# Optimization experiments

Hardware: AMD Instinct MI355X
Metric: run time of the kernel (lower is better)

The kernel has to match this reference:

```python
import jax, jax.numpy as jnp
import numpy as np

B, NF, V, D, NI = 16384, 26, 100000, 16, 13
HID = [512, 256, 128, 64, 1]

def setup_inputs() -> dict:
    key = jax.random.key(0)
    ks = jax.random.split(key, 24)
    x_int = jax.random.normal(ks[0], (B, NI), dtype=jnp.float32)
    x_cat = jax.random.randint(ks[1], (B, NF), 0, V, dtype=jnp.int64)
    emb_tables = jax.random.normal(ks[2], (NF, V, D), dtype=jnp.float32) * 0.01
    lin_tables = jax.random.normal(ks[3], (NF, V, 1), dtype=jnp.float32) * 0.01
    W_num = jax.random.normal(ks[4], (NI, 1), dtype=jnp.float32) * 0.1
    b_num = jnp.zeros((1,), dtype=jnp.float32)
    bias = jnp.zeros((1,), dtype=jnp.float32)
    dims = [NF * D + NI] + HID  # 429 -> 512 -> 256 -> 128 -> 64 -> 1
    mlp = {}
    for li in range(5):
        fan_in = dims[li]
        mlp[f'W{li+1}'] = jax.random.normal(ks[5 + 2*li], (dims[li], dims[li+1]), dtype=jnp.float32) / np.sqrt(fan_in)
        mlp[f'b{li+1}'] = jnp.zeros((dims[li+1],), dtype=jnp.float32)
    return dict(x_int=x_int, x_cat=x_cat, emb_tables=emb_tables, lin_tables=lin_tables,
                W_num=W_num, b_num=b_num, bias=bias, **mlp)

def reference(x_int, x_cat, emb_tables, lin_tables, W_num, b_num, bias,
              W1, b1, W2, b2, W3, b3, W4, b4, W5, b5):
    feat_idx = jnp.arange(NF)[None, :]                 # [1, NF]
    emb = emb_tables[feat_idx, x_cat]                  # [B, NF, D] fused gather
    # FM second-order interaction
    sum_emb = jnp.sum(emb, axis=1)                     # [B, D]
    square_of_sum = sum_emb ** 2
    sum_of_square = jnp.sum(emb ** 2, axis=1)
    fm_score = 0.5 * jnp.sum(square_of_sum - sum_of_square, axis=1, keepdims=True)  # [B,1]
    # linear terms
    lin_cat_score = jnp.sum(lin_tables[feat_idx, x_cat], axis=1)  # [B,1]
    lin_num_score = x_int @ W_num + b_num                          # [B,1]
    # deep MLP (dropout is identity at inference)
    deep_in = jnp.concatenate([emb.reshape(emb.shape[0], -1), x_int], axis=1)  # [B, NF*D+NI]
    h = jax.nn.relu(deep_in @ W1 + b1)
    h = jax.nn.relu(h @ W2 + b2)
    h = jax.nn.relu(h @ W3 + b3)
    h = jax.nn.relu(h @ W4 + b4)
    deep_score = h @ W5 + b5                                       # [B,1]
    return bias + lin_cat_score + lin_num_score + fm_score + deep_score
```

## Files before the change

kernel.cpp:

```cpp
#include <hip/hip_runtime.h>
#include <hip/hip_bf16.h>
#include <stdint.h>

typedef __bf16 bf16x8 __attribute__((ext_vector_type(8)));
typedef float  f32x4  __attribute__((ext_vector_type(4)));

#define NROWS 16384
#define NFEAT 26
#define VOCAB 100000

template<int KPAD, int KREAL, int N, int NCT, int WS>
__device__ __forceinline__ void mlp_layer(const float* __restrict__ W,
                                          const float* __restrict__ bias,
                                          const __bf16* Ain, __bf16* Aout,
                                          int w, int lane) {
  constexpr int LDA = KPAD + 8, LDO = N + 8;
  constexpr int KSAFE = (KREAL / 32) * 32;
  const int lrow = lane & 15;
  const int kg = (lane >> 4) * 8;

  f32x4 acc[NCT][4];
  #pragma unroll
  for (int j = 0; j < NCT; ++j)
    #pragma unroll
    for (int m = 0; m < 4; ++m)
      #pragma unroll
      for (int i = 0; i < 4; ++i) acc[j][m][i] = 0.f;

  int col[NCT];
  #pragma unroll
  for (int j = 0; j < NCT; ++j) col[j] = (w + j * WS) * 16 + lrow;

  auto step = [&](int k0, bool clamp) {
    bf16x8 af[4];
    #pragma unroll
    for (int m = 0; m < 4; ++m)
      af[m] = *(const bf16x8*)(Ain + (m * 16 + lrow) * LDA + k0 + kg);
    #pragma unroll
    for (int j = 0; j < NCT; ++j) {
      bf16x8 bf;
      #pragma unroll
      for (int i = 0; i < 8; ++i) {
        int k = k0 + kg + i;
        float v = (!clamp || k < KREAL) ? W[(size_t)k * N + col[j]] : 0.f;
        bf[i] = (__bf16)v;
      }
      #pragma unroll
      for (int m = 0; m < 4; ++m)
        acc[j][m] = __builtin_amdgcn_mfma_f32_16x16x32_bf16(af[m], bf, acc[j][m], 0, 0, 0);
    }
  };

  for (int k0 = 0; k0 < KSAFE; k0 += 32) step(k0, false);
  if constexpr (KSAFE < KPAD) step(KSAFE, true);

  const int rbase = (lane >> 4) * 4;
  #pragma unroll
  for (int j = 0; j < NCT; ++j) {
    float bv = bias[col[j]];
    #pragma unroll
    for (int m = 0; m < 4; ++m)
      #pragma unroll
      for (int i = 0; i < 4; ++i) {
        float v = acc[j][m][i] + bv;
        v = fmaxf(v, 0.f);
        Aout[(m * 16 + rbase + i) * LDO + col[j]] = (__bf16)v;
      }
  }
}

__global__ __launch_bounds__(1024) void k_fused(
    const float* __restrict__ x_int,
    const int*   __restrict__ x_cat,
    const float* __restrict__ emb,
    const float* __restrict__ lin,
    const float* __restrict__ W_num,
    const float* __restrict__ b_num,
    const float* __restrict__ bias0,
    const float* __restrict__ W1, const float* __restrict__ b1,
    const float* __restrict__ W2, const float* __restrict__ b2,
    const float* __restrict__ W3, const float* __restrict__ b3,
    const float* __restrict__ W4, const float* __restrict__ b4,
    const float* __restrict__ W5, const float* __restrict__ b5,
    float* __restrict__ out) {
  __shared__ __align__(16) char smem[125184];
  __bf16* A0 = (__bf16*)smem;
  __bf16* A1 = (__bf16*)(smem + 58368);
  int* s_idx = (int*)(smem + 58368);
  float* s_part = (float*)(smem + 124928);

  const int t = threadIdx.x;
  const int row0 = blockIdx.x * 64;
  const int w = t >> 6, lane = t & 63;

  for (int i = t; i < 64 * NFEAT; i += 1024) {
    int r = i / NFEAT, f = i - r * NFEAT;
    s_idx[i] = x_cat[(size_t)(row0 + r) * NFEAT + f];
  }
  __syncthreads();

  {
    const float pbias = bias0[0] + b_num[0];
    const int r = t >> 4, d = t & 15;
    float sum = 0.f, sumsq = 0.f;
    #pragma unroll
    for (int f = 0; f < NFEAT; ++f) {
      int idx = s_idx[r * NFEAT + f];
      float e = emb[((size_t)f * VOCAB + idx) * 16 + d];
      sum += e; sumsq += e * e;
      A0[r * 456 + f * 16 + d] = (__bf16)e;
    }
    float xv = (d < 13) ? x_int[(size_t)(row0 + r) * 13 + d] : 0.f;
    A0[r * 456 + 416 + d] = (__bf16)xv;
    A0[r * 456 + 432 + d] = (__bf16)0.f;

    float lin_s = lin[(size_t)d * VOCAB + s_idx[r * NFEAT + d]];
    if (d < NFEAT - 16)
      lin_s += lin[(size_t)(d + 16) * VOCAB + s_idx[r * NFEAT + d + 16]];
    float lin_num = (d < 13) ? xv * W_num[d] : 0.f;

    float red = 0.5f * (sum * sum - sumsq) + lin_s + lin_num;
    #pragma unroll
    for (int off = 1; off < 16; off <<= 1) red += __shfl_xor(red, off, 16);
    if (d == 0) s_part[r] = red + pbias;
  }
  __syncthreads();

  mlp_layer<448, 429, 512, 2, 16>(W1, b1, A0, A1, w, lane);
  __syncthreads();
  mlp_layer<512, 512, 256, 1, 16>(W2, b2, A1, A0, w, lane);
  __syncthreads();
  if (w < 8) mlp_layer<256, 256, 128, 1, 8>(W3, b3, A0, A1, w, lane);
  __syncthreads();
  if (w < 4) mlp_layer<128, 128, 64, 1, 4>(W4, b4, A1, A0, w, lane);
  __syncthreads();

  {
    const int r = t >> 4, g = t & 15;
    float s = 0.f;
    #pragma unroll
    for (int i = 0; i < 4; ++i)
      s += (float)A0[r * 72 + g * 4 + i] * W5[g * 4 + i];
    #pragma unroll
    for (int off = 1; off < 16; off <<= 1) s += __shfl_xor(s, off, 16);
    if (g == 0) out[row0 + r] = s + b5[0] + s_part[r];
  }
}

extern "C" void kernel_launch(void* const* d_in, const int* in_sizes, int n_in,
                              void* d_out, int out_size, void* d_ws, size_t ws_size,
                              hipStream_t stream) {
  const float* x_int = (const float*)d_in[0];
  const int*   x_cat = (const int*)d_in[1];
  const float* emb   = (const float*)d_in[2];
  const float* lin   = (const float*)d_in[3];
  const float* W_num = (const float*)d_in[4];
  const float* b_num = (const float*)d_in[5];
  const float* bias  = (const float*)d_in[6];
  const float* W1 = (const float*)d_in[7];  const float* b1 = (const float*)d_in[8];
  const float* W2 = (const float*)d_in[9];  const float* b2 = (const float*)d_in[10];
  const float* W3 = (const float*)d_in[11]; const float* b3 = (const float*)d_in[12];
  const float* W4 = (const float*)d_in[13]; const float* b4 = (const float*)d_in[14];
  const float* W5 = (const float*)d_in[15]; const float* b5 = (const float*)d_in[16];
  float* out = (float*)d_out;

  k_fused<<<NROWS / 64, 1024, 0, stream>>>(x_int, x_cat, emb, lin, W_num, b_num, bias,
                                           W1, b1, W2, b2, W3, b3, W4, b4, W5, b5,
                                           out);
}
```

Baseline: 46.46 us.

## Interleave embedding gather with first MLP layer in feature chunks

The embedding gather and the first MLP layer now run chunk by chunk: each chunk of four features (64 columns) is written to shared memory, then fed to the bf16 MFMA accumulation for layer 1. Meanwhile the next chunk's gather is prefetched with 16-byte vector loads. The aim is to hide the latency of the random embedding reads behind matrix-core work, instead of finishing the whole gather before layer 1 starts. The FM and linear reductions are rebuilt around the new thread mapping. The cost is seven block-wide barriers inside the loop and more live registers.

New measurement: 44.17 us. 1.05x faster.

```diff
diff --git a/kernel.cpp b/kernel.cpp
--- a/kernel.cpp
+++ b/kernel.cpp
@@ -3,6 +3,7 @@
 #include <stdint.h>
 
 typedef __bf16 bf16x8 __attribute__((ext_vector_type(8)));
+typedef __bf16 bf16x4 __attribute__((ext_vector_type(4)));
 typedef float  f32x4  __attribute__((ext_vector_type(4)));
 
 #define NROWS 16384
@@ -15,7 +16,6 @@
                                           const __bf16* Ain, __bf16* Aout,
                                           int w, int lane) {
   constexpr int LDA = KPAD + 8, LDO = N + 8;
-  constexpr int KSAFE = (KREAL / 32) * 32;
   const int lrow = lane & 15;
   const int kg = (lane >> 4) * 8;
 
@@ -31,28 +31,22 @@
   #pragma unroll
   for (int j = 0; j < NCT; ++j) col[j] = (w + j * WS) * 16 + lrow;
 
-  auto step = [&](int k0, bool clamp) {
+  for (int k0 = 0; k0 < KREAL; k0 += 32) {
     bf16x8 af[4];
     #pragma unroll
     for (int m = 0; m < 4; ++m)
       af[m] = *(const bf16x8*)(Ain + (m * 16 + lrow) * LDA + k0 + kg);
     #pragma unroll
     for (int j = 0; j < NCT; ++j) {
-      bf16x8 bf;
-      #pragma unroll
-      for (int i = 0; i < 8; ++i) {
-        int k = k0 + kg + i;
-        float v = (!clamp || k < KREAL) ? W[(size_t)k * N + col[j]] : 0.f;
-        bf[i] = (__bf16)v;
-      }
+      bf16x8 bw;
+      #pragma unroll
+      for (int i = 0; i < 8; ++i)
+        bw[i] = (__bf16)W[(size_t)(k0 + kg + i) * N + col[j]];
       #pragma unroll
       for (int m = 0; m < 4; ++m)
-        acc[j][m] = __builtin_amdgcn_mfma_f32_16x16x32_bf16(af[m], bf, acc[j][m], 0, 0, 0);
-    }
-  };
-
-  for (int k0 = 0; k0 < KSAFE; k0 += 32) step(k0, false);
-  if constexpr (KSAFE < KPAD) step(KSAFE, true);
+        acc[j][m] = __builtin_amdgcn_mfma_f32_16x16x32_bf16(af[m], bw, acc[j][m], 0, 0, 0);
+    }
+  }
 
   const int rbase = (lane >> 4) * 4;
   #pragma unroll
@@ -92,6 +86,7 @@
   const int t = threadIdx.x;
   const int row0 = blockIdx.x * 64;
   const int w = t >> 6, lane = t & 63;
+  const int lrow = lane & 15, kg = (lane >> 4) * 8;
 
   for (int i = t; i < 64 * NFEAT; i += 1024) {
     int r = i / NFEAT, f = i - r * NFEAT;
@@ -99,35 +94,127 @@
   }
   __syncthreads();
 
-  {
-    const float pbias = bias0[0] + b_num[0];
-    const int r = t >> 4, d = t & 15;
-    float sum = 0.f, sumsq = 0.f;
-    #pragma unroll
-    for (int f = 0; f < NFEAT; ++f) {
-      int idx = s_idx[r * NFEAT + f];
-      float e = emb[((size_t)f * VOCAB + idx) * 16 + d];
-      sum += e; sumsq += e * e;
-      A0[r * 456 + f * 16 + d] = (__bf16)e;
-    }
-    float xv = (d < 13) ? x_int[(size_t)(row0 + r) * 13 + d] : 0.f;
-    A0[r * 456 + 416 + d] = (__bf16)xv;
-    A0[r * 456 + 432 + d] = (__bf16)0.f;
-
-    float lin_s = lin[(size_t)d * VOCAB + s_idx[r * NFEAT + d]];
-    if (d < NFEAT - 16)
-      lin_s += lin[(size_t)(d + 16) * VOCAB + s_idx[r * NFEAT + d + 16]];
-    float lin_num = (d < 13) ? xv * W_num[d] : 0.f;
-
-    float red = 0.5f * (sum * sum - sumsq) + lin_s + lin_num;
-    #pragma unroll
-    for (int off = 1; off < 16; off <<= 1) red += __shfl_xor(red, off, 16);
-    if (d == 0) s_part[r] = red + pbias;
-  }
-  __syncthreads();
-
-  mlp_layer<448, 429, 512, 2, 16>(W1, b1, A0, A1, w, lane);
-  __syncthreads();
+  const int r = t >> 4, d = t & 15;
+  const int g = d >> 2, q = d & 3;
+
+  float lin_s = 0.f;
+  if (d < 13) {
+    lin_s = lin[(size_t)d * VOCAB + s_idx[r * NFEAT + d]]
+          + lin[(size_t)(d + 13) * VOCAB + s_idx[r * NFEAT + d + 13]]
+          + x_int[(size_t)(row0 + r) * 13 + d] * W_num[d];
+  }
+  float xv[4] = {0.f, 0.f, 0.f, 0.f};
+  if (d >= 8 && d < 12) {
+    int base = (d - 8) * 4;
+    #pragma unroll
+    for (int i = 0; i < 4; ++i)
+      if (base + i < 13) xv[i] = x_int[(size_t)(row0 + r) * 13 + base + i];
+  }
+
+  f32x4 acc[2][4];
+  #pragma unroll
+  for (int j = 0; j < 2; ++j)
+    #pragma unroll
+    for (int m = 0; m < 4; ++m)
+      #pragma unroll
+      for (int i = 0; i < 4; ++i) acc[j][m][i] = 0.f;
+  const int colL1[2] = { w * 16 + lrow, (w + 16) * 16 + lrow };
+
+  float fsum[4] = {0.f,0.f,0.f,0.f}, fsq[4] = {0.f,0.f,0.f,0.f};
+  f32x4 cur;
+  {
+    int idx = s_idx[r * NFEAT + g];
+    cur = *(const f32x4*)(emb + ((size_t)g * VOCAB + idx) * 16 + q * 4);
+  }
+
+  #pragma unroll
+  for (int c = 0; c < 7; ++c) {
+    f32x4 nxt;
+    if (c < 6) {
+      int fc = 4 * (c + 1) + g;
+      if (fc < NFEAT) {
+        int idx = s_idx[r * NFEAT + fc];
+        nxt = *(const f32x4*)(emb + ((size_t)fc * VOCAB + idx) * 16 + q * 4);
+      }
+    }
+    const int colbase = c * 64 + g * 16 + q * 4;
+    if (4 * c + g < NFEAT) {
+      bf16x4 pk;
+      #pragma unroll
+      for (int i = 0; i < 4; ++i) {
+        fsum[i] += cur[i]; fsq[i] += cur[i] * cur[i];
+        pk[i] = (__bf16)cur[i];
+      }
+      *(bf16x4*)(A0 + r * 456 + colbase) = pk;
+    } else {
+      bf16x4 pk;
+      #pragma unroll
+      for (int i = 0; i < 4; ++i) pk[i] = (__bf16)xv[i];
+      *(bf16x4*)(A0 + r * 456 + colbase) = pk;
+    }
+    asm volatile("s_waitcnt lgkmcnt(0)" ::: "memory");
+    __builtin_amdgcn_s_barrier();
+    asm volatile("" ::: "memory");
+    #pragma unroll
+    for (int ks = 0; ks < 2; ++ks) {
+      const int k0 = c * 64 + ks * 32;
+      bf16x8 af[4];
+      #pragma unroll
+      for (int m = 0; m < 4; ++m)
+        af[m] = *(const bf16x8*)(A0 + (m * 16 + lrow) * 456 + k0 + kg);
+      #pragma unroll
+      for (int j = 0; j < 2; ++j) {
+        bf16x8 bw;
+        #pragma unroll
+        for (int i = 0; i < 8; ++i) {
+          int k = k0 + kg + i;
+          float v;
+          if (c < 6) v = W1[(size_t)k * 512 + colL1[j]];
+          else       v = (k < 429) ? W1[(size_t)k * 512 + colL1[j]] : 0.f;
+          bw[i] = (__bf16)v;
+        }
+        #pragma unroll
+        for (int m = 0; m < 4; ++m)
+          acc[j][m] = __builtin_amdgcn_mfma_f32_16x16x32_bf16(af[m], bw, acc[j][m], 0, 0, 0);
+      }
+    }
+    cur = nxt;
+  }
+
+  {
+    const int rbase = (lane >> 4) * 4;
+    #pragma unroll
+    for (int j = 0; j < 2; ++j) {
+      float bv = b1[colL1[j]];
+      #pragma unroll
+      for (int m = 0; m < 4; ++m)
+        #pragma unroll
+        for (int i = 0; i < 4; ++i) {
+          float v = acc[j][m][i] + bv;
+          v = fmaxf(v, 0.f);
+          A1[(m * 16 + rbase + i) * 520 + colL1[j]] = (__bf16)v;
+        }
+    }
+  }
+
+  {
+    #pragma unroll
+    for (int i = 0; i < 4; ++i) {
+      fsum[i] += __shfl_xor(fsum[i], 4); fsq[i] += __shfl_xor(fsq[i], 4);
+      fsum[i] += __shfl_xor(fsum[i], 8); fsq[i] += __shfl_xor(fsq[i], 8);
+    }
+    float fmq = 0.f;
+    #pragma unroll
+    for (int i = 0; i < 4; ++i) fmq += fsum[i] * fsum[i] - fsq[i];
+    fmq += __shfl_xor(fmq, 1);
+    fmq += __shfl_xor(fmq, 2);
+    float linred = lin_s;
+    #pragma unroll
+    for (int off = 1; off < 16; off <<= 1) linred += __shfl_xor(linred, off, 16);
+    if (d == 0) s_part[r] = 0.5f * fmq + linred + bias0[0] + b_num[0];
+  }
+  __syncthreads();
+
   mlp_layer<512, 512, 256, 1, 16>(W2, b2, A1, A0, w, lane);
   __syncthreads();
   if (w < 8) mlp_layer<256, 256, 128, 1, 8>(W3, b3, A0, A1, w, lane);
@@ -136,14 +223,14 @@
   __syncthreads();
 
   {
-    const int r = t >> 4, g = t & 15;
+    const int rr = t >> 4, gg = t & 15;
     float s = 0.f;
     #pragma unroll
     for (int i = 0; i < 4; ++i)
-      s += (float)A0[r * 72 + g * 4 + i] * W5[g * 4 + i];
+      s += (float)A0[rr * 72 + gg * 4 + i] * W5[gg * 4 + i];
     #pragma unroll
     for (int off = 1; off < 16; off <<= 1) s += __shfl_xor(s, off, 16);
-    if (g == 0) out[row0 + r] = s + b5[0] + s_part[r];
+    if (gg == 0) out[row0 + rr] = s + b5[0] + s_part[rr];
   }
 }
 
```
